# Performance work log

Hardware: AMD Instinct MI355X
Metric: run time of the kernel (lower is better)

The kernel has to match this reference:

```python
import jax, jax.numpy as jnp
from jax import lax
import numpy as np

B, T, I, H = 64, 2048, 256, 256


def setup_inputs() -> dict:
    key = jax.random.key(0)
    k_x, k_h, k_wi, k_bi, k_wh, k_bh = jax.random.split(key, 6)
    si = 1.0 / np.sqrt(I)
    sh = 1.0 / np.sqrt(H)
    return {
        "x": jax.random.normal(k_x, (B, T, I), dtype=jnp.float32),
        "h0": jax.random.normal(k_h, (B, H), dtype=jnp.float32),
        "W_ih": jax.random.uniform(k_wi, (3 * H, I), dtype=jnp.float32, minval=-si, maxval=si),
        "b_ih": jax.random.uniform(k_bi, (3 * H,), dtype=jnp.float32, minval=-si, maxval=si),
        "W_hh": jax.random.uniform(k_wh, (3 * H, H), dtype=jnp.float32, minval=-sh, maxval=sh),
        "b_hh": jax.random.uniform(k_bh, (3 * H,), dtype=jnp.float32, minval=-sh, maxval=sh),
    }


def reference(x, h0, W_ih, b_ih, W_hh, b_hh):
    # batch_first=True -> transpose to time-major [T, B, I]
    xt = jnp.transpose(x, (1, 0, 2))
    # Batch the input-to-hidden projection across all timesteps (one big GEMM)
    gi = jnp.einsum("tbi,gi->tbg", xt, W_ih) + b_ih  # [T, B, 3H]

    def step(h, gi_t):
        gh = h @ W_hh.T + b_hh                     # [B, 3H]
        i_r, i_c, i_u = jnp.split(gi_t, 3, axis=1)
        h_r, h_c, h_u = jnp.split(gh, 3, axis=1)
        u = jax.nn.sigmoid(i_u + h_u)              # update gate
        r = jax.nn.sigmoid(i_r + h_r)              # reset gate
        n = jnp.tanh(i_c + r * h_c)                # candidate state
        hy = (1.0 - u) * h + u * n
        return hy, hy

    hN, out = lax.scan(step, h0, gi)               # out: [T, B, H]
    return jnp.transpose(out, (1, 0, 2)), hN       # ([B, T, H], [B, H])
```

## Files before the change

kernel.cpp:

```cpp
#include <hip/hip_runtime.h>
#include <cstdint>
#include <cstddef>

#define B_ 64
#define T_ 2048
#define I_ 256
#define H_ 256
#define G_ 768

typedef _Float16 h2v __attribute__((ext_vector_type(2)));
typedef _Float16 v8h __attribute__((ext_vector_type(8)));
typedef float    v4f __attribute__((ext_vector_type(4)));
typedef uint32_t u32x4 __attribute__((ext_vector_type(4)));

union U32h { uint32_t u; h2v h; };
__device__ __forceinline__ h2v asH(uint32_t u) { U32h t; t.u = u; return t.h; }

__global__ void prep_whh2(const float* __restrict__ Whh, uint32_t* __restrict__ Wprep) {
    int j = threadIdx.x;
    int gh = blockIdx.x;
    int g = gh >> 1, half = gh & 1;
    const float* src = Whh + (size_t)(g * 256 + j) * 256 + half * 128;
    uint32_t* dst = Wprep + ((size_t)gh * 256 + j) * 64;
    for (int p = 0; p < 64; ++p) {
        U32h u; u.h = h2v{(_Float16)src[2 * p], (_Float16)src[2 * p + 1]};
        dst[p] = u.u;
    }
}

#define LDA 56
#define LDB 56

__launch_bounds__(256, 2)
__global__ void gemm_gi(const float* __restrict__ x, const float* __restrict__ Wih,
                        const float* __restrict__ bih, _Float16* __restrict__ gi,
                        int t0) {
    __shared__ __align__(16) _Float16 As[64 * LDA];
    __shared__ __align__(16) _Float16 Bs[384 * LDB];
    int tid  = threadIdx.x;
    int t    = t0 + blockIdx.x;
    int n0   = blockIdx.y * 384;
    int lane = tid & 63, wave = tid >> 6;
    int quad = lane >> 4, r16 = lane & 15;

    v4f acc[24];
#pragma unroll
    for (int i = 0; i < 24; ++i) acc[i] = v4f{0.f, 0.f, 0.f, 0.f};

    for (int ki = 0; ki < 8; ++ki) {
        int k0 = ki * 32;
        __syncthreads();
#pragma unroll
        for (int s = 0; s < 2; ++s) {
            int slot = tid + s * 256;
            int row = slot >> 3;
            int part = slot & 7;
            const float* xp = x + ((size_t)row * T_ + t) * I_ + k0 + part * 4;
            float4 v = *(const float4*)xp;
            U32h u0, u1;
            u0.h = h2v{(_Float16)v.x, (_Float16)v.y};
            u1.h = h2v{(_Float16)v.z, (_Float16)v.w};
            uint32_t* dst = (uint32_t*)&As[row * LDA + part * 4];
            dst[0] = u0.u; dst[1] = u1.u;
        }
#pragma unroll
        for (int s = 0; s < 12; ++s) {
            int slot = tid + s * 256;
            int row = slot >> 3;
            int part = slot & 7;
            const float* wp = Wih + (size_t)(n0 + row) * I_ + k0 + part * 4;
            float4 v = *(const float4*)wp;
            U32h u0, u1;
            u0.h = h2v{(_Float16)v.x, (_Float16)v.y};
            u1.h = h2v{(_Float16)v.z, (_Float16)v.w};
            uint32_t* dst = (uint32_t*)&Bs[row * LDB + part * 4];
            dst[0] = u0.u; dst[1] = u1.u;
        }
        __syncthreads();
        v8h af = *(const v8h*)&As[(wave * 16 + r16) * LDA + quad * 8];
#pragma unroll
        for (int nt = 0; nt < 24; ++nt) {
            v8h bf = *(const v8h*)&Bs[(nt * 16 + r16) * LDB + quad * 8];
            acc[nt] = __builtin_amdgcn_mfma_f32_16x16x32_f16(af, bf, acc[nt], 0, 0, 0);
        }
    }
#pragma unroll
    for (int nt = 0; nt < 24; ++nt) {
        int n = n0 + nt * 16 + r16;
        float bias = bih[n];
#pragma unroll
        for (int reg = 0; reg < 4; ++reg) {
            int m = wave * 16 + quad * 4 + reg;
            size_t off = ((size_t)blockIdx.x * 64 + m) * G_ + n;
            gi[off] = (_Float16)(acc[nt][reg] + bias);
        }
    }
}

__launch_bounds__(512, 2)
__global__ void rec_step(const uint32_t* __restrict__ Wprep, const float* __restrict__ bhh,
                         const _Float16* __restrict__ gi, const float* __restrict__ h_init,
                         float* __restrict__ out, float* __restrict__ hN,
                         float* __restrict__ h_carry, int t0, int len) {
    __shared__ __align__(16) _Float16 hb[2][256];
    __shared__ float part[2][3][256];

    int b = blockIdx.x;
    int tid = threadIdx.x;
    int j = tid & 255, half = tid >> 8;

    const u32x4* wp0 = (const u32x4*)(Wprep + ((size_t)(0 * 2 + half) * 256 + j) * 64);
    const u32x4* wp1 = (const u32x4*)(Wprep + ((size_t)(1 * 2 + half) * 256 + j) * 64);
    const u32x4* wp2 = (const u32x4*)(Wprep + ((size_t)(2 * 2 + half) * 256 + j) * 64);
    u32x4 wq0[16], wq1[16], wq2[16];
#pragma unroll
    for (int p = 0; p < 16; ++p) wq0[p] = wp0[p];
#pragma unroll
    for (int p = 0; p < 16; ++p) wq1[p] = wp1[p];
#pragma unroll
    for (int p = 0; p < 16; ++p) wq2[p] = wp2[p];

    float bh0 = 0.f, bh1 = 0.f, bh2 = 0.f, hprev = 0.f;
    float g0 = 0.f, g1 = 0.f, g2 = 0.f;
    const _Float16* gp = gi + (size_t)b * G_ + j;
    float* outp = out + (size_t)b * T_ * H_ + (size_t)t0 * H_ + j;
    if (tid < 256) {
        bh0 = bhh[j]; bh1 = bhh[256 + j]; bh2 = bhh[512 + j];
        hprev = h_init[b * 256 + j];
        hb[0][j] = (_Float16)hprev;
        g0 = (float)gp[0]; g1 = (float)gp[256]; g2 = (float)gp[512];
    }
    __syncthreads();

    int cur = 0;
    for (int t = 0; t < len; ++t) {
        float p0 = 0.f, p1 = 0.f, p2 = 0.f;
        if (tid < 256 && t + 1 < len) {
            const _Float16* gq = gp + (size_t)(t + 1) * B_ * G_;
            p0 = (float)gq[0]; p1 = (float)gq[256]; p2 = (float)gq[512];
        }

        float a0 = 0.f, a1 = 0.f, a2 = 0.f;
        const u32x4* hv4 = (const u32x4*)&hb[cur][half * 128];
#pragma unroll
        for (int p4 = 0; p4 < 16; ++p4) {
            u32x4 hv = hv4[p4];
#pragma unroll
            for (int q = 0; q < 4; ++q) {
                h2v hq = asH(hv[q]);
                a0 = __builtin_amdgcn_fdot2(asH(wq0[p4][q]), hq, a0, false);
                a1 = __builtin_amdgcn_fdot2(asH(wq1[p4][q]), hq, a1, false);
                a2 = __builtin_amdgcn_fdot2(asH(wq2[p4][q]), hq, a2, false);
            }
        }
        part[half][0][j] = a0;
        part[half][1][j] = a1;
        part[half][2][j] = a2;
        __syncthreads();

        if (tid < 256) {
            float s0 = part[0][0][j] + part[1][0][j] + bh0;
            float s1 = part[0][1][j] + part[1][1][j] + bh1;
            float s2 = part[0][2][j] + part[1][2][j] + bh2;
            float r = 1.f / (1.f + __expf(-(g0 + s0)));
            float u = 1.f / (1.f + __expf(-(g2 + s2)));
            float carg = g1 + r * s1;
            carg = fminf(fmaxf(carg, -20.f), 20.f);
            float e2 = __expf(2.f * carg);
            float n = (e2 - 1.f) / (e2 + 1.f);
            float hnew = hprev + u * (n - hprev);
            outp[(size_t)t * H_] = hnew;
            hb[cur ^ 1][j] = (_Float16)hnew;
            hprev = hnew;
            g0 = p0; g1 = p1; g2 = p2;
        }
        __syncthreads();
        cur ^= 1;
    }
    if (tid < 256) {
        h_carry[b * 256 + j] = hprev;
        if (t0 + len == T_) hN[b * 256 + j] = hprev;
    }
}

extern "C" void kernel_launch(void* const* d_in, const int* in_sizes, int n_in,
                              void* d_out, int out_size, void* d_ws, size_t ws_size,
                              hipStream_t stream) {
    const float* x   = (const float*)d_in[0];
    const float* h0  = (const float*)d_in[1];
    const float* Wih = (const float*)d_in[2];
    const float* bih = (const float*)d_in[3];
    const float* Whh = (const float*)d_in[4];
    const float* bhh = (const float*)d_in[5];
    float* out = (float*)d_out;
    float* hN  = out + (size_t)B_ * T_ * H_;

    char* ws = (char*)d_ws;
    float*    h_carry = (float*)ws;
    uint32_t* Wprep   = (uint32_t*)(ws + 65536);
    _Float16* gi      = (_Float16*)(ws + 65536 + 393216);

    const size_t head = 65536 + 393216;
    const size_t per_t = (size_t)B_ * G_ * sizeof(_Float16);
    size_t avail = (ws_size > head) ? (ws_size - head) : 0;
    int tc = (int)(avail / per_t);
    if (tc > T_) tc = T_;
    if (tc < 1)  tc = 1;
    int nch = (T_ + tc - 1) / tc;
    tc = (T_ + nch - 1) / nch;

    hipLaunchKernelGGL(prep_whh2, dim3(6), dim3(256), 0, stream, Whh, Wprep);
    for (int t0 = 0; t0 < T_; t0 += tc) {
        int len = (T_ - t0 < tc) ? (T_ - t0) : tc;
        hipLaunchKernelGGL(gemm_gi, dim3(len, 2), dim3(256), 0, stream,
                           x, Wih, bih, gi, t0);
        const float* hi = (t0 == 0) ? h0 : h_carry;
        hipLaunchKernelGGL(rec_step, dim3(64), dim3(512), 0, stream,
                           Wprep, bhh, gi, hi, out, hN, h_carry, t0, len);
    }
}
```

Measured before the change: 2.976 ms.

## Use MFMA for recurrent matvec with register-resident W_hh fragments

Replaces the per-thread fdot2 recurrent matvec with MFMA 16x16x32 instructions. W_hh is pre-packed into MFMA A-fragment layout and kept in registers, and h is broadcast as the B operand. Only column 0 of each MFMA result is used, so most of the MFMA work is wasted, but the approach cuts per-step instruction count and removes the two-half partial-sum reduction. Launch bounds change to one block per CU because of the larger register footprint.

```diff
diff --git a/kernel.cpp b/kernel.cpp
--- a/kernel.cpp
+++ b/kernel.cpp
@@ -14,18 +14,19 @@
 typedef uint32_t u32x4 __attribute__((ext_vector_type(4)));
 
 union U32h { uint32_t u; h2v h; };
-__device__ __forceinline__ h2v asH(uint32_t u) { U32h t; t.u = u; return t.h; }
-
-__global__ void prep_whh2(const float* __restrict__ Whh, uint32_t* __restrict__ Wprep) {
-    int j = threadIdx.x;
-    int gh = blockIdx.x;
-    int g = gh >> 1, half = gh & 1;
-    const float* src = Whh + (size_t)(g * 256 + j) * 256 + half * 128;
-    uint32_t* dst = Wprep + ((size_t)gh * 256 + j) * 64;
-    for (int p = 0; p < 64; ++p) {
+
+__global__ void prep_whh_frag(const float* __restrict__ Whh, uint32_t* __restrict__ Wp) {
+    int rt = blockIdx.x;
+    int kb = blockIdx.y;
+    int lane = threadIdx.x;
+    int r16 = lane & 15, hi2 = lane >> 4;
+    const float* src = Whh + (size_t)(rt * 16 + r16) * 256 + kb * 32 + hi2 * 8;
+    uint32_t d[4];
+    for (int p = 0; p < 4; ++p) {
         U32h u; u.h = h2v{(_Float16)src[2 * p], (_Float16)src[2 * p + 1]};
-        dst[p] = u.u;
-    }
+        d[p] = u.u;
+    }
+    *(u32x4*)(Wp + (((size_t)rt * 8 + kb) * 64 + lane) * 4) = u32x4{d[0], d[1], d[2], d[3]};
 }
 
 #define LDA 56
@@ -97,28 +98,27 @@
     }
 }
 
-__launch_bounds__(512, 2)
-__global__ void rec_step(const uint32_t* __restrict__ Wprep, const float* __restrict__ bhh,
-                         const _Float16* __restrict__ gi, const float* __restrict__ h_init,
-                         float* __restrict__ out, float* __restrict__ hN,
-                         float* __restrict__ h_carry, int t0, int len) {
+__global__ void __launch_bounds__(512, 1)
+rec_step(const v8h* __restrict__ Wfrag, const float* __restrict__ bhh,
+         const _Float16* __restrict__ gi, const float* __restrict__ h_init,
+         float* __restrict__ out, float* __restrict__ hN,
+         float* __restrict__ h_carry, int t0, int len) {
     __shared__ __align__(16) _Float16 hb[2][256];
-    __shared__ float part[2][3][256];
+    __shared__ __align__(16) float ypart[G_];
 
     int b = blockIdx.x;
     int tid = threadIdx.x;
-    int j = tid & 255, half = tid >> 8;
-
-    const u32x4* wp0 = (const u32x4*)(Wprep + ((size_t)(0 * 2 + half) * 256 + j) * 64);
-    const u32x4* wp1 = (const u32x4*)(Wprep + ((size_t)(1 * 2 + half) * 256 + j) * 64);
-    const u32x4* wp2 = (const u32x4*)(Wprep + ((size_t)(2 * 2 + half) * 256 + j) * 64);
-    u32x4 wq0[16], wq1[16], wq2[16];
-#pragma unroll
-    for (int p = 0; p < 16; ++p) wq0[p] = wp0[p];
-#pragma unroll
-    for (int p = 0; p < 16; ++p) wq1[p] = wp1[p];
-#pragma unroll
-    for (int p = 0; p < 16; ++p) wq2[p] = wp2[p];
+    int lane = tid & 63, wave = tid >> 6;
+    int r16 = lane & 15, hi2 = lane >> 4;
+    int j = tid & 255;
+
+    v8h w[48];
+#pragma unroll
+    for (int f = 0; f < 48; ++f) {
+        int rt = wave * 6 + (f >> 3);
+        int kb = f & 7;
+        w[f] = Wfrag[((size_t)rt * 8 + kb) * 64 + lane];
+    }
 
     float bh0 = 0.f, bh1 = 0.f, bh2 = 0.f, hprev = 0.f;
     float g0 = 0.f, g1 = 0.f, g2 = 0.f;
@@ -140,28 +140,26 @@
             p0 = (float)gq[0]; p1 = (float)gq[256]; p2 = (float)gq[512];
         }
 
-        float a0 = 0.f, a1 = 0.f, a2 = 0.f;
-        const u32x4* hv4 = (const u32x4*)&hb[cur][half * 128];
-#pragma unroll
-        for (int p4 = 0; p4 < 16; ++p4) {
-            u32x4 hv = hv4[p4];
-#pragma unroll
-            for (int q = 0; q < 4; ++q) {
-                h2v hq = asH(hv[q]);
-                a0 = __builtin_amdgcn_fdot2(asH(wq0[p4][q]), hq, a0, false);
-                a1 = __builtin_amdgcn_fdot2(asH(wq1[p4][q]), hq, a1, false);
-                a2 = __builtin_amdgcn_fdot2(asH(wq2[p4][q]), hq, a2, false);
-            }
-        }
-        part[half][0][j] = a0;
-        part[half][1][j] = a1;
-        part[half][2][j] = a2;
+        v8h bf[8];
+#pragma unroll
+        for (int kb = 0; kb < 8; ++kb)
+            bf[kb] = *(const v8h*)&hb[cur][kb * 32 + hi2 * 8];
+
+#pragma unroll
+        for (int r = 0; r < 6; ++r) {
+            v4f acc = v4f{0.f, 0.f, 0.f, 0.f};
+#pragma unroll
+            for (int kb = 0; kb < 8; ++kb)
+                acc = __builtin_amdgcn_mfma_f32_16x16x32_f16(w[r * 8 + kb], bf[kb], acc, 0, 0, 0);
+            if (r16 == 0)
+                *(v4f*)&ypart[(wave * 6 + r) * 16 + hi2 * 4] = acc;
+        }
         __syncthreads();
 
         if (tid < 256) {
-            float s0 = part[0][0][j] + part[1][0][j] + bh0;
-            float s1 = part[0][1][j] + part[1][1][j] + bh1;
-            float s2 = part[0][2][j] + part[1][2][j] + bh2;
+            float s0 = ypart[j]       + bh0;
+            float s1 = ypart[256 + j] + bh1;
+            float s2 = ypart[512 + j] + bh2;
             float r = 1.f / (1.f + __expf(-(g0 + s0)));
             float u = 1.f / (1.f + __expf(-(g2 + s2)));
             float carg = g1 + r * s1;
@@ -209,13 +207,13 @@
     int nch = (T_ + tc - 1) / tc;
     tc = (T_ + nch - 1) / nch;
 
-    hipLaunchKernelGGL(prep_whh2, dim3(6), dim3(256), 0, stream, Whh, Wprep);
+    hipLaunchKernelGGL(prep_whh_frag, dim3(48, 8), dim3(64), 0, stream, Whh, Wprep);
     for (int t0 = 0; t0 < T_; t0 += tc) {
         int len = (T_ - t0 < tc) ? (T_ - t0) : tc;
         hipLaunchKernelGGL(gemm_gi, dim3(len, 2), dim3(256), 0, stream,
                            x, Wih, bih, gi, t0);
         const float* hi = (t0 == 0) ? h0 : h_carry;
         hipLaunchKernelGGL(rec_step, dim3(64), dim3(512), 0, stream,
-                           Wprep, bhh, gi, hi, out, hN, h_carry, t0, len);
-    }
-}
+                           (const v8h*)Wprep, bhh, gi, hi, out, hN, h_carry, t0, len);
+    }
+}
```

Result: slower. 3.144 ms (+5.6%).
